# Kernel tuning notes

Measured on AMD Instinct MI355X. Metric: run time of the kernel, lower is better.

The kernel has to match this reference:

```python
import jax, jax.numpy as jnp
import numpy as np

N, E, D_IN, H, C = 50000, 1200000, 128, 8, 8  # heads=8, per-head dim=8, hidden=64
EPS_BN = 1e-5


def _bn(x, g, b):
    # BatchNorm1d in training mode: per-feature batch mean / biased var
    m = x.mean(0)
    v = x.var(0)
    return g * (x - m) * jax.lax.rsqrt(v + EPS_BN) + b


def _gatv2(x, src, dst, Wl, Wr, att):
    # PyG GATv2Conv (concat=True, bias=False, negative_slope=0.2, eval-mode dropout)
    xl = (x @ Wl).reshape(N, H, C)  # source transform (lin_l)
    xr = (x @ Wr).reshape(N, H, C)  # target transform (lin_r)
    e = jax.nn.leaky_relu(xl[src] + xr[dst], 0.2)          # [E,H,C]
    logits = jnp.einsum('ehc,hc->eh', e, att)               # [E,H]
    mx = jax.ops.segment_max(logits, dst, num_segments=N)   # [N,H]
    ex = jnp.exp(logits - mx[dst])
    den = jax.ops.segment_sum(ex, dst, num_segments=N)      # [N,H]
    alpha = ex / (den[dst] + 1e-16)                         # segment softmax over in-edges
    msg = xl[src] * alpha[..., None]                        # [E,H,C]
    out = jax.ops.segment_sum(msg.reshape(E, H * C), dst, num_segments=N)
    return out  # [N,64]


def setup_inputs() -> dict:
    key = jax.random.key(0)
    ks = jax.random.split(key, 40)
    d = {}
    d['x'] = jax.random.normal(ks[0], (N, D_IN), dtype=jnp.float32)
    d['edge_index'] = jax.random.randint(ks[1], (2, E), 0, N, dtype=jnp.int64)
    d['Wpre'] = jax.random.normal(ks[2], (D_IN, 64), dtype=jnp.float32) * 0.05
    d['g0'] = jnp.ones((64,), jnp.float32); d['b0'] = jnp.zeros((64,), jnp.float32)
    for i, k0 in zip(range(1, 5), range(3, 19, 4)):
        d[f'Wl{i}'] = jax.random.normal(ks[k0], (64, 64), jnp.float32) * 0.1
        d[f'Wr{i}'] = jax.random.normal(ks[k0 + 1], (64, 64), jnp.float32) * 0.1
        d[f'att{i}'] = jax.random.normal(ks[k0 + 2], (H, C), jnp.float32) * 0.1
        d[f'g{i}'] = jnp.ones((64,), jnp.float32)
        d[f'b{i}'] = jnp.zeros((64,), jnp.float32)
    dims = [64, 48, 32, 16, 2]
    for j in range(4):
        d[f'Wp{j+1}'] = jax.random.normal(ks[20 + j], (dims[j], dims[j + 1]), jnp.float32) * 0.1
        d[f'bp{j+1}'] = jnp.zeros((dims[j + 1],), jnp.float32)
    return d


def reference(x, edge_index, Wpre, g0, b0,
              Wl1, Wr1, att1, g1, b1,
              Wl2, Wr2, att2, g2, b2,
              Wl3, Wr3, att3, g3, b3,
              Wl4, Wr4, att4, g4, b4,
              Wp1, bp1, Wp2, bp2, Wp3, bp3, Wp4, bp4):
    src, dst = edge_index[0], edge_index[1]
    h = jax.nn.elu(_bn(x @ Wpre, g0, b0))
    for Wl, Wr, att, g, b in ((Wl1, Wr1, att1, g1, b1),
                              (Wl2, Wr2, att2, g2, b2),
                              (Wl3, Wr3, att3, g3, b3),
                              (Wl4, Wr4, att4, g4, b4)):
        h = jax.nn.elu(_bn(_gatv2(h, src, dst, Wl, Wr, att) + h, g, b))
    h = jax.nn.elu(h @ Wp1 + bp1)
    h = jax.nn.elu(h @ Wp2 + bp2)
    h = jax.nn.elu(h @ Wp3 + bp3)
    return h @ Wp4 + bp4
```

## Files before the change

### kernel.cpp

```cpp
#include <hip/hip_runtime.h>
#include <hip/hip_bf16.h>
#include <cmath>

__device__ inline void unpack_bf2(unsigned int u, float& lo, float& hi) {
    union { unsigned int i; float f; } a, b;
    a.i = u << 16; b.i = u & 0xffff0000u;
    lo = a.f; hi = b.f;
}
__device__ inline unsigned short bf16_bits(float x) {
    __hip_bfloat16 v = __float2bfloat16(x);
    return *reinterpret_cast<unsigned short*>(&v);
}

template<int K, int M, int ROWS>
__global__ __launch_bounds__(256)
void bn_gemm_kernel(const float* __restrict__ A, const float* __restrict__ B0,
                    const float* __restrict__ B1, float* __restrict__ C,
                    __hip_bfloat16* __restrict__ xlb, __hip_bfloat16* __restrict__ xrb,
                    const float* __restrict__ stats, const float* __restrict__ g,
                    const float* __restrict__ b, float* __restrict__ part,
                    int N, float invN)
{
    constexpr int TM  = ROWS * M / 512;
    constexpr int LDA = K + 4;
    constexpr int MT  = M / TM;
    __shared__ float Bs[K * M];
    __shared__ float As[ROWS * LDA];
    __shared__ float sA[K], sB[K];
    __shared__ float pst[2][4][64];
    if (stats != nullptr && threadIdx.x < K) {
        float m   = stats[threadIdx.x] * invN;
        float var = stats[K + threadIdx.x] * invN - m * m;
        float a   = g[threadIdx.x] * rsqrtf(var + 1e-5f);
        sA[threadIdx.x] = a;
        sB[threadIdx.x] = b[threadIdx.x] - m * a;
    }
    for (int i = threadIdx.x; i < K * M; i += 256) {
        float v;
        if (B1 != nullptr) {
            int k = i / M, m = i - k * M;
            v = (m < M / 2) ? B0[k * (M / 2) + m] : B1[k * (M / 2) + (m - M / 2)];
        } else {
            v = B0[i];
        }
        Bs[i] = v;
    }
    __syncthreads();
    int row0 = blockIdx.x * ROWS;
    for (int i = threadIdx.x; i < ROWS * K; i += 256) {
        int rr = i / K, kk = i - rr * K;
        int r = row0 + rr;
        float v = (r < N) ? A[(size_t)r * K + kk] : 0.f;
        if (stats != nullptr) {
            float t = fmaf(v, sA[kk], sB[kk]);
            v = (t > 0.f) ? t : expm1f(t);
        }
        As[rr * LDA + kk] = v;
    }
    __syncthreads();
    int r0 = (threadIdx.x / MT) * 2;
    int m0 = (threadIdx.x % MT) * TM;
    float acc0[TM], acc1[TM];
    #pragma unroll
    for (int i = 0; i < TM; ++i) { acc0[i] = 0.f; acc1[i] = 0.f; }
    const float* a0p = &As[r0 * LDA];
    const float* a1p = a0p + LDA;
    for (int k = 0; k < K; ++k) {
        float a0 = a0p[k], a1 = a1p[k];
        #pragma unroll
        for (int mm = 0; mm < TM; mm += 4) {
            float4 bv = *(const float4*)&Bs[k * M + m0 + mm];
            acc0[mm + 0] = fmaf(a0, bv.x, acc0[mm + 0]);
            acc0[mm + 1] = fmaf(a0, bv.y, acc0[mm + 1]);
            acc0[mm + 2] = fmaf(a0, bv.z, acc0[mm + 2]);
            acc0[mm + 3] = fmaf(a0, bv.w, acc0[mm + 3]);
            acc1[mm + 0] = fmaf(a1, bv.x, acc1[mm + 0]);
            acc1[mm + 1] = fmaf(a1, bv.y, acc1[mm + 1]);
            acc1[mm + 2] = fmaf(a1, bv.z, acc1[mm + 2]);
            acc1[mm + 3] = fmaf(a1, bv.w, acc1[mm + 3]);
        }
    }
    int rA = row0 + r0, rB = rA + 1;
    if (C != nullptr) {
        #pragma unroll
        for (int mm = 0; mm < TM; mm += 4) {
            if (rA < N)
                *(float4*)&C[(size_t)rA * M + m0 + mm] =
                    make_float4(acc0[mm], acc0[mm+1], acc0[mm+2], acc0[mm+3]);
            if (rB < N)
                *(float4*)&C[(size_t)rB * M + m0 + mm] =
                    make_float4(acc1[mm], acc1[mm+1], acc1[mm+2], acc1[mm+3]);
        }
    } else {
        unsigned int u0[4], u1[4];
        #pragma unroll
        for (int i = 0; i < 4; ++i) {
            u0[i] = (unsigned int)bf16_bits(acc0[2*i]) |
                    ((unsigned int)bf16_bits(acc0[2*i+1]) << 16);
            u1[i] = (unsigned int)bf16_bits(acc1[2*i]) |
                    ((unsigned int)bf16_bits(acc1[2*i+1]) << 16);
        }
        __hip_bfloat16* dst = (m0 < 64) ? xlb : xrb;
        int mo = (m0 < 64) ? m0 : m0 - 64;
        if (rA < N) *(uint4*)(dst + (size_t)rA * 64 + mo) = make_uint4(u0[0],u0[1],u0[2],u0[3]);
        if (rB < N) *(uint4*)(dst + (size_t)rB * 64 + mo) = make_uint4(u1[0],u1[1],u1[2],u1[3]);
    }
    if (part != nullptr) {
        float s[TM], s2[TM];
        #pragma unroll
        for (int i = 0; i < TM; ++i) {
            s[i]  = acc0[i] + acc1[i];
            s2[i] = acc0[i] * acc0[i] + acc1[i] * acc1[i];
        }
        #pragma unroll
        for (int off = MT; off < 64; off <<= 1) {
            #pragma unroll
            for (int i = 0; i < TM; ++i) {
                s[i]  += __shfl_xor(s[i],  off);
                s2[i] += __shfl_xor(s2[i], off);
            }
        }
        int lane = threadIdx.x & 63, wid = threadIdx.x >> 6;
        if (lane < MT) {
            #pragma unroll
            for (int c = 0; c < TM; ++c) {
                pst[0][wid][lane * TM + c] = s[c];
                pst[1][wid][lane * TM + c] = s2[c];
            }
        }
        __syncthreads();
        if (threadIdx.x < 128) {
            int which = threadIdx.x >> 6, f = threadIdx.x & 63;
            part[(size_t)blockIdx.x * 128 + threadIdx.x] =
                pst[which][0][f] + pst[which][1][f] +
                pst[which][2][f] + pst[which][3][f];
        }
    }
}

__global__ __launch_bounds__(128)
void stats_reduce1_kernel(const float* __restrict__ part, int nb,
                          float* __restrict__ part2)
{
    int f = threadIdx.x;
    float s = 0.f;
    for (int r = blockIdx.x; r < nb; r += 64)
        s += part[(size_t)r * 128 + f];
    part2[(size_t)blockIdx.x * 128 + f] = s;
}

__global__ __launch_bounds__(128)
void stats_reduce2_kernel(const float* __restrict__ part2,
                          float* __restrict__ stats)
{
    int f = threadIdx.x;
    float a = 0.f;
    #pragma unroll 8
    for (int r = 0; r < 64; ++r)
        a += part2[(size_t)r * 128 + f];
    stats[f] = a;
}

__global__ __launch_bounds__(256)
void bin_hist_kernel(const int* __restrict__ dsts, int* __restrict__ binCnt, int E)
{
    __shared__ int lh[4][256];
    for (int i = threadIdx.x; i < 1024; i += 256) ((int*)lh)[i] = 0;
    __syncthreads();
    int bank = threadIdx.x & 3;
    for (int e0 = blockIdx.x * 1024 + threadIdx.x * 4; e0 < E; e0 += gridDim.x * 1024) {
        if (e0 + 3 < E) {
            int4 d = *(const int4*)&dsts[e0];
            atomicAdd(&lh[bank][d.x >> 8], 1);
            atomicAdd(&lh[bank][d.y >> 8], 1);
            atomicAdd(&lh[bank][d.z >> 8], 1);
            atomicAdd(&lh[bank][d.w >> 8], 1);
        } else {
            for (int j = 0; j < 4; ++j)
                if (e0 + j < E) atomicAdd(&lh[bank][dsts[e0 + j] >> 8], 1);
        }
    }
    __syncthreads();
    int s = lh[0][threadIdx.x] + lh[1][threadIdx.x] +
            lh[2][threadIdx.x] + lh[3][threadIdx.x];
    if (s > 0) atomicAdd(&binCnt[threadIdx.x], s);
}

__global__ __launch_bounds__(256)
void bin_scan_kernel(const int* __restrict__ binCnt, int* __restrict__ binBase,
                     int* __restrict__ binCursor, int* __restrict__ row_ptr,
                     int* __restrict__ col, int N, int E)
{
    __shared__ int buf[256];
    int v = binCnt[threadIdx.x];
    buf[threadIdx.x] = v;
    __syncthreads();
    for (int off = 1; off < 256; off <<= 1) {
        int t = (threadIdx.x >= off) ? buf[threadIdx.x - off] : 0;
        __syncthreads();
        buf[threadIdx.x] += t;
        __syncthreads();
    }
    int excl = buf[threadIdx.x] - v;
    binBase[threadIdx.x] = excl;
    binCursor[threadIdx.x] = excl;
    if (threadIdx.x < 64) col[E + threadIdx.x] = 0;
    if (threadIdx.x == 255) {
        binBase[256] = buf[255];
        row_ptr[N] = E;
    }
}

#define SCHUNK 4096
__global__ __launch_bounds__(256)
void bin_scatter_kernel(const int* __restrict__ srcs, const int* __restrict__ dsts,
                        int* __restrict__ binCursor, unsigned int* __restrict__ binned,
                        int E)
{
    __shared__ unsigned int stg[SCHUNK];
    __shared__ int bcnt[256], bexcl[256], bcur[256], gbase[256], sbuf[256];
    int c0 = blockIdx.x * SCHUNK;
    int n = min(SCHUNK, E - c0);
    bcnt[threadIdx.x] = 0;
    __syncthreads();
    for (int k = 0; k < SCHUNK / 256; ++k) {
        int i = c0 + k * 256 + threadIdx.x;
        if (i < E) atomicAdd(&bcnt[dsts[i] >> 8], 1);
    }
    __syncthreads();
    int v = bcnt[threadIdx.x];
    sbuf[threadIdx.x] = v;
    __syncthreads();
    for (int off = 1; off < 256; off <<= 1) {
        int t = (threadIdx.x >= off) ? sbuf[threadIdx.x - off] : 0;
        __syncthreads();
        sbuf[threadIdx.x] += t;
        __syncthreads();
    }
    bexcl[threadIdx.x] = sbuf[threadIdx.x] - v;
    bcur[threadIdx.x]  = sbuf[threadIdx.x] - v;
    __syncthreads();
    for (int k = 0; k < SCHUNK / 256; ++k) {
        int i = c0 + k * 256 + threadIdx.x;
        if (i < E) {
            unsigned int s = (unsigned int)srcs[i], d = (unsigned int)dsts[i];
            int pos = atomicAdd(&bcur[d >> 8], 1);
            stg[pos] = (s << 16) | d;
        }
    }
    __syncthreads();
    gbase[threadIdx.x] = atomicAdd(&binCursor[threadIdx.x], bcnt[threadIdx.x]);
    __syncthreads();
    for (int i = threadIdx.x; i < n; i += 256) {
        unsigned int p = stg[i];
        int b = (p & 0xFFFFu) >> 8;
        binned[gbase[b] + (i - bexcl[b])] = p;
    }
}

__global__ __launch_bounds__(256)
void bin_finalize_kernel(const unsigned int* __restrict__ binned,
                         const int* __restrict__ binBase,
                         int* __restrict__ row_ptr, int* __restrict__ col, int N)
{
    __shared__ int cnt[256], excl[256], cur[256];
    int b = blockIdx.x;
    int beg = binBase[b], end = binBase[b + 1];
    cnt[threadIdx.x] = 0;
    __syncthreads();
    for (int i = beg + threadIdx.x; i < end; i += 256)
        atomicAdd(&cnt[binned[i] & 255u], 1);
    __syncthreads();
    int v = cnt[threadIdx.x];
    excl[threadIdx.x] = v;
    __syncthreads();
    for (int off = 1; off < 256; off <<= 1) {
        int t = (threadIdx.x >= off) ? excl[threadIdx.x - off] : 0;
        __syncthreads();
        excl[threadIdx.x] += t;
        __syncthreads();
    }
    int ex = excl[threadIdx.x] - v;
    int dstIdx = b * 256 + threadIdx.x;
    if (dstIdx < N) row_ptr[dstIdx] = beg + ex;
    cur[threadIdx.x] = ex;
    __syncthreads();
    for (int i = beg + threadIdx.x; i < end; i += 256) {
        unsigned int p = binned[i];
        int pos = atomicAdd(&cur[p & 255u], 1);
        col[beg + pos] = (int)(p >> 16) << 7;
    }
}

__device__ inline uint4 ldrow(const char* base_h, int offv, int slot) {
    int off = __shfl(offv, slot);
    return *(const uint4*)(base_h + off);
}

__global__ __launch_bounds__(256)
void gat_node_kernel(const int* __restrict__ row_ptr, const int* __restrict__ coloff,
                     const __hip_bfloat16* __restrict__ xlb,
                     const __hip_bfloat16* __restrict__ xrb,
                     const float* __restrict__ att,
                     const float* __restrict__ zin,
                     const float* __restrict__ stats, const float* __restrict__ g,
                     const float* __restrict__ b,
                     float* __restrict__ zout, float* __restrict__ part,
                     int N, float invN)
{
    int lane = threadIdx.x & 63;
    int wid  = threadIdx.x >> 6;
    int eg   = lane >> 3;
    int h    = lane & 7;

    __shared__ float AB[2][64];
    if (threadIdx.x < 64) {
        float m   = stats[threadIdx.x] * invN;
        float var = stats[64 + threadIdx.x] * invN - m * m;
        float a   = g[threadIdx.x] * rsqrtf(var + 1e-5f);
        AB[0][threadIdx.x] = a;
        AB[1][threadIdx.x] = b[threadIdx.x] - m * a;
    }
    __syncthreads();

    float attv[8];
    {
        const float4* a4 = (const float4*)(att + (h << 3));
        float4 a0 = a4[0], a1 = a4[1];
        attv[0]=a0.x; attv[1]=a0.y; attv[2]=a0.z; attv[3]=a0.w;
        attv[4]=a1.x; attv[5]=a1.y; attv[6]=a1.z; attv[7]=a1.w;
    }
    float fs[8], fs2[8];
    #pragma unroll
    for (int c = 0; c < 8; ++c) { fs[c] = 0.f; fs2[c] = 0.f; }

    const char* xh = (const char*)xlb + (h << 4);
    const int stride = gridDim.x * 4;

    int n = blockIdx.x * 4 + wid;
    int beg = 0, end = 0, cv0 = 0;
    if (n < N) {
        beg = row_ptr[n]; end = row_ptr[n + 1];
        int mm = min(lane, end - beg - 1); if (mm < 0) mm = 0;
        cv0 = coloff[beg + mm];
    }
    while (n < N) {
        uint4 xrp = *(const uint4*)((const char*)xrb + (size_t)n * 128 + (h << 4));
        float xr[8];
        unpack_bf2(xrp.x, xr[0], xr[1]);
        unpack_bf2(xrp.y, xr[2], xr[3]);
        unpack_bf2(xrp.z, xr[4], xr[5]);
        unpack_bf2(xrp.w, xr[6], xr[7]);
        float acc[8];
        #pragma unroll
        for (int c = 0; c < 8; ++c) acc[c] = 0.f;
        float den = 0.f;

        for (int gb = beg; gb < end; gb += 64) {
            int cnt = min(64, end - gb);
            int cm1 = cnt - 1;
            int cv = (gb == beg) ? cv0 : coloff[gb + min(lane, cm1)];
            int nck = (cnt + 15) >> 4;
            uint4 pA = ldrow(xh, cv, min(eg, cm1));
            uint4 pB = ldrow(xh, cv, min(eg + 8, cm1));
            for (int c = 0; c < nck; ++c) {
                uint4 nA = pA, nB = pB;
                if (c + 1 < nck) {
                    nA = ldrow(xh, cv, min((c + 1) * 16 + eg,     cm1));
                    nB = ldrow(xh, cv, min((c + 1) * 16 + 8 + eg, cm1));
                }
                int s0 = c * 16 + eg, s1 = s0 + 8;
                {
                    float xl[8];
                    unpack_bf2(pA.x, xl[0], xl[1]);
                    unpack_bf2(pA.y, xl[2], xl[3]);
                    unpack_bf2(pA.z, xl[4], xl[5]);
                    unpack_bf2(pA.w, xl[6], xl[7]);
                    float logit = 0.f;
                    #pragma unroll
                    for (int cc = 0; cc < 8; ++cc) {
                        float sum = xl[cc] + xr[cc];
                        float lr = fmaxf(sum, 0.2f * sum);
                        logit = fmaf(lr, attv[cc], logit);
                    }
                    float ex = (s0 < cnt) ? __expf(logit) : 0.f;
                    #pragma unroll
                    for (int cc = 0; cc < 8; ++cc) acc[cc] = fmaf(ex, xl[cc], acc[cc]);
                    den += ex;
                }
                {
                    float xl[8];
                    unpack_bf2(pB.x, xl[0], xl[1]);
                    unpack_bf2(pB.y, xl[2], xl[3]);
                    unpack_bf2(pB.z, xl[4], xl[5]);
                    unpack_bf2(pB.w, xl[6], xl[7]);
                    float logit = 0.f;
                    #pragma unroll
                    for (int cc = 0; cc < 8; ++cc) {
                        float sum = xl[cc] + xr[cc];
                        float lr = fmaxf(sum, 0.2f * sum);
                        logit = fmaf(lr, attv[cc], logit);
                    }
                    float ex = (s1 < cnt) ? __expf(logit) : 0.f;
                    #pragma unroll
                    for (int cc = 0; cc < 8; ++cc) acc[cc] = fmaf(ex, xl[cc], acc[cc]);
                    den += ex;
                }
                pA = nA; pB = nB;
            }
        }
        int n2 = n + stride;
        int beg2 = 0, end2 = 0;
        if (n2 < N) { beg2 = row_ptr[n2]; end2 = row_ptr[n2 + 1]; }
        float4 hr0, hr1;
        if (eg == 0) {
            const float4* zp = (const float4*)(zin + (size_t)n * 64 + (h << 3));
            hr0 = zp[0]; hr1 = zp[1];
        }
        #pragma unroll
        for (int off = 8; off <= 32; off <<= 1) {
            den += __shfl_xor(den, off);
            #pragma unroll
            for (int c = 0; c < 8; ++c) acc[c] += __shfl_xor(acc[c], off);
        }
        int cv2 = 0;
        if (n2 < N) {
            int mm = min(lane, end2 - beg2 - 1); if (mm < 0) mm = 0;
            cv2 = coloff[beg2 + mm];
        }
        if (eg == 0) {
            float inv = 1.f / (den + 1e-16f);
            float hraw[8] = {hr0.x, hr0.y, hr0.z, hr0.w, hr1.x, hr1.y, hr1.z, hr1.w};
            float v[8];
            #pragma unroll
            for (int c = 0; c < 8; ++c) {
                int f = (h << 3) + c;
                float t = fmaf(hraw[c], AB[0][f], AB[1][f]);
                float hv = (t > 0.f) ? t : expm1f(t);
                v[c] = fmaf(acc[c], inv, hv);
                fs[c] += v[c];
                fs2[c] += v[c] * v[c];
            }
            float4* z4 = (float4*)(zout + (size_t)n * 64 + (h << 3));
            z4[0] = make_float4(v[0], v[1], v[2], v[3]);
            z4[1] = make_float4(v[4], v[5], v[6], v[7]);
        }
        n = n2; beg = beg2; end = end2; cv0 = cv2;
    }
    __shared__ float lstat[2][4][64];
    if (eg == 0) {
        #pragma unroll
        for (int c = 0; c < 8; ++c) {
            lstat[0][wid][(h << 3) + c] = fs[c];
            lstat[1][wid][(h << 3) + c] = fs2[c];
        }
    }
    __syncthreads();
    if (threadIdx.x < 128) {
        int which = threadIdx.x >> 6;
        int f = threadIdx.x & 63;
        part[(size_t)blockIdx.x * 128 + threadIdx.x] =
            lstat[which][0][f] + lstat[which][1][f] +
            lstat[which][2][f] + lstat[which][3][f];
    }
}

__device__ inline float elu_f(float t) { return (t > 0.f) ? t : expm1f(t); }

__global__ __launch_bounds__(256)
void mlp_kernel(const float* __restrict__ z, const float* __restrict__ stats,
                const float* __restrict__ g, const float* __restrict__ b,
                const float* __restrict__ W1, const float* __restrict__ B1,
                const float* __restrict__ W2, const float* __restrict__ B2,
                const float* __restrict__ W3, const float* __restrict__ B3,
                const float* __restrict__ W4, const float* __restrict__ B4,
                float* __restrict__ out, int N, float invN)
{
    __shared__ float w1[64 * 48], w2[48 * 32], w3[32 * 16], w4[16 * 2];
    __shared__ float bb1[48], bb2[32], bb3[16], bb4[2];
    __shared__ float sA[64], sB[64];
    for (int i = threadIdx.x; i < 64 * 48; i += 256) w1[i] = W1[i];
    for (int i = threadIdx.x; i < 48 * 32; i += 256) w2[i] = W2[i];
    for (int i = threadIdx.x; i < 32 * 16; i += 256) w3[i] = W3[i];
    for (int i = threadIdx.x; i < 16 * 2;  i += 256) w4[i] = W4[i];
    if (threadIdx.x < 48) bb1[threadIdx.x] = B1[threadIdx.x];
    if (threadIdx.x < 32) bb2[threadIdx.x] = B2[threadIdx.x];
    if (threadIdx.x < 16) bb3[threadIdx.x] = B3[threadIdx.x];
    if (threadIdx.x < 2)  bb4[threadIdx.x] = B4[threadIdx.x];
    if (threadIdx.x >= 64 && threadIdx.x < 128) {
        int f = threadIdx.x - 64;
        float m   = stats[f] * invN;
        float var = stats[64 + f] * invN - m * m;
        float a   = g[f] * rsqrtf(var + 1e-5f);
        sA[f] = a;
        sB[f] = b[f] - m * a;
    }
    __syncthreads();
    int n = blockIdx.x * 256 + threadIdx.x;
    if (n >= N) return;
    float a[64];
    const float4* hp = (const float4*)(z + (size_t)n * 64);
    #pragma unroll
    for (int i = 0; i < 16; ++i) {
        float4 v = hp[i];
        a[4 * i] = v.x; a[4 * i + 1] = v.y; a[4 * i + 2] = v.z; a[4 * i + 3] = v.w;
    }
    #pragma unroll
    for (int k = 0; k < 64; ++k)
        a[k] = elu_f(fmaf(a[k], sA[k], sB[k]));

    float t1[48];
    for (int j = 0; j < 48; j += 4) {
        float c0 = bb1[j], c1 = bb1[j+1], c2 = bb1[j+2], c3 = bb1[j+3];
        #pragma unroll
        for (int k = 0; k < 64; ++k) {
            float4 wv = *(const float4*)&w1[k * 48 + j];
            c0 = fmaf(a[k], wv.x, c0);
            c1 = fmaf(a[k], wv.y, c1);
            c2 = fmaf(a[k], wv.z, c2);
            c3 = fmaf(a[k], wv.w, c3);
        }
        t1[j] = elu_f(c0); t1[j+1] = elu_f(c1); t1[j+2] = elu_f(c2); t1[j+3] = elu_f(c3);
    }
    float t2[32];
    for (int j = 0; j < 32; j += 4) {
        float c0 = bb2[j], c1 = bb2[j+1], c2 = bb2[j+2], c3 = bb2[j+3];
        #pragma unroll
        for (int k = 0; k < 48; ++k) {
            float4 wv = *(const float4*)&w2[k * 32 + j];
            c0 = fmaf(t1[k], wv.x, c0);
            c1 = fmaf(t1[k], wv.y, c1);
            c2 = fmaf(t1[k], wv.z, c2);
            c3 = fmaf(t1[k], wv.w, c3);
        }
        t2[j] = elu_f(c0); t2[j+1] = elu_f(c1); t2[j+2] = elu_f(c2); t2[j+3] = elu_f(c3);
    }
    float t3[16];
    for (int j = 0; j < 16; j += 4) {
        float c0 = bb3[j], c1 = bb3[j+1], c2 = bb3[j+2], c3 = bb3[j+3];
        #pragma unroll
        for (int k = 0; k < 32; ++k) {
            float4 wv = *(const float4*)&w3[k * 16 + j];
            c0 = fmaf(t2[k], wv.x, c0);
            c1 = fmaf(t2[k], wv.y, c1);
            c2 = fmaf(t2[k], wv.z, c2);
            c3 = fmaf(t2[k], wv.w, c3);
        }
        t3[j] = elu_f(c0); t3[j+1] = elu_f(c1); t3[j+2] = elu_f(c2); t3[j+3] = elu_f(c3);
    }
    float o0 = bb4[0], o1 = bb4[1];
    #pragma unroll
    for (int k = 0; k < 16; ++k) {
        o0 += t3[k] * w4[k * 2 + 0];
        o1 += t3[k] * w4[k * 2 + 1];
    }
    out[(size_t)n * 2 + 0] = o0;
    out[(size_t)n * 2 + 1] = o1;
}

extern "C" void kernel_launch(void* const* d_in, const int* in_sizes, int n_in,
                              void* d_out, int out_size, void* d_ws, size_t ws_size,
                              hipStream_t stream)
{
    const float* x    = (const float*)d_in[0];
    const int*   ei   = (const int*)d_in[1];
    const float* Wpre = (const float*)d_in[2];
    const float* g0   = (const float*)d_in[3];
    const float* b0   = (const float*)d_in[4];

    const int N = in_sizes[0] / 128;
    const int E = in_sizes[1] / 2;
    const float invN = 1.f / (float)N;
    const int NB = (N + 255) >> 8;
    const int GB = (N + 31) / 32;
    const int GG = 2048;

    float* ws  = (float*)d_ws;
    float* zA  = ws;
    float* zB  = zA + (size_t)N * 64;
    __hip_bfloat16* xlb = (__hip_bfloat16*)(zB + (size_t)N * 64);
    __hip_bfloat16* xrb = xlb + (size_t)N * 64;
    float* stats   = (float*)(xrb + (size_t)N * 64);
    int*   row_ptr = (int*)(stats + 5 * 128);
    int*   col     = row_ptr + N + 4;
    int*   binCnt    = col + E + 64;
    int*   binBase   = binCnt + 256;
    int*   binCursor = binBase + 260;
    float* part    = (float*)(binCursor + 256);
    float* part2   = part + (size_t)2048 * 128;
    unsigned int* binned = (unsigned int*)zB;

    const int* srcs = ei;
    const int* dsts = ei + E;

    hipMemsetAsync(binCnt, 0, 256 * sizeof(int), stream);
    bin_hist_kernel<<<256, 256, 0, stream>>>(dsts, binCnt, E);
    bin_scan_kernel<<<1, 256, 0, stream>>>(binCnt, binBase, binCursor, row_ptr, col, N, E);
    bin_scatter_kernel<<<(E + SCHUNK - 1) / SCHUNK, 256, 0, stream>>>(
        srcs, dsts, binCursor, binned, E);
    bin_finalize_kernel<<<NB, 256, 0, stream>>>(binned, binBase, row_ptr, col, N);

    bn_gemm_kernel<128, 64, 32><<<GB, 256, 0, stream>>>(
        x, Wpre, nullptr, zA, nullptr, nullptr, nullptr, nullptr, nullptr,
        part, N, invN);
    stats_reduce1_kernel<<<64, 128, 0, stream>>>(part, GB, part2);
    stats_reduce2_kernel<<<1, 128, 0, stream>>>(part2, stats);

    for (int l = 0; l < 4; ++l) {
        const float* Wl  = (const float*)d_in[5 + 5 * l + 0];
        const float* Wr  = (const float*)d_in[5 + 5 * l + 1];
        const float* att = (const float*)d_in[5 + 5 * l + 2];
        const float* gp = (l == 0) ? g0 : (const float*)d_in[5 + 5 * (l - 1) + 3];
        const float* bp = (l == 0) ? b0 : (const float*)d_in[5 + 5 * (l - 1) + 4];
        float* statsp = stats + 128 * l;
        float* zin  = (l & 1) ? zB : zA;
        float* zout = (l & 1) ? zA : zB;

        bn_gemm_kernel<64, 128, 32><<<GB, 256, 0, stream>>>(
            zin, Wl, Wr, nullptr, xlb, xrb, statsp, gp, bp, nullptr, N, invN);
        gat_node_kernel<<<GG, 256, 0, stream>>>(
            row_ptr, col, xlb, xrb, att, zin, statsp, gp, bp,
            zout, part, N, invN);
        stats_reduce1_kernel<<<64, 128, 0, stream>>>(part, GG, part2);
        stats_reduce2_kernel<<<1, 128, 0, stream>>>(part2, stats + 128 * (l + 1));
    }

    const float* g4  = (const float*)d_in[23];
    const float* b4  = (const float*)d_in[24];
    const float* Wp1 = (const float*)d_in[25]; const float* bp1 = (const float*)d_in[26];
    const float* Wp2 = (const float*)d_in[27]; const float* bp2 = (const float*)d_in[28];
    const float* Wp3 = (const float*)d_in[29]; const float* bp3 = (const float*)d_in[30];
    const float* Wp4 = (const float*)d_in[31]; const float* bp4 = (const float*)d_in[32];
    mlp_kernel<<<(N + 255) / 256, 256, 0, stream>>>(
        zA, stats + 512, g4, b4, Wp1, bp1, Wp2, bp2, Wp3, bp3, Wp4, bp4,
        (float*)d_out, N, invN);
}
```

Measured before the change: 517.7 us.

## Split final MLP across four lanes per node with shuffle-based activation exchange

The final MLP kernel now assigns four threads to each node instead of one. Each lane holds a quarter of the input features and computes a quarter of every layer's outputs, and the full activation vector is gathered via warp shuffles. This is meant to cut per-thread register pressure (previously 64+48+32+16 floats) and raise occupancy and parallelism. In exchange it adds shuffle traffic and launches four times as many threads. Only lane 0 of each group writes the output, as a single float2 store.

New measurement: 740.9 us. 43.1% more time.

```diff
diff --git a/kernel.cpp b/kernel.cpp
--- a/kernel.cpp
+++ b/kernel.cpp
@@ -496,66 +496,97 @@
         sB[f] = b[f] - m * a;
     }
     __syncthreads();
-    int n = blockIdx.x * 256 + threadIdx.x;
+    int t = blockIdx.x * 256 + threadIdx.x;
+    int n = t >> 2;
     if (n >= N) return;
-    float a[64];
-    const float4* hp = (const float4*)(z + (size_t)n * 64);
-    #pragma unroll
-    for (int i = 0; i < 16; ++i) {
-        float4 v = hp[i];
-        a[4 * i] = v.x; a[4 * i + 1] = v.y; a[4 * i + 2] = v.z; a[4 * i + 3] = v.w;
-    }
-    #pragma unroll
-    for (int k = 0; k < 64; ++k)
-        a[k] = elu_f(fmaf(a[k], sA[k], sB[k]));
-
-    float t1[48];
-    for (int j = 0; j < 48; j += 4) {
-        float c0 = bb1[j], c1 = bb1[j+1], c2 = bb1[j+2], c3 = bb1[j+3];
+    int lane = threadIdx.x & 63;
+    int q    = lane & 3;
+    int base = lane & ~3;
+
+    float a[16];
+    {
+        const float4* hp = (const float4*)(z + (size_t)n * 64 + (q << 4));
+        #pragma unroll
+        for (int i = 0; i < 4; ++i) {
+            float4 v = hp[i];
+            a[4*i] = v.x; a[4*i+1] = v.y; a[4*i+2] = v.z; a[4*i+3] = v.w;
+        }
+        #pragma unroll
+        for (int i = 0; i < 16; ++i) {
+            int f = (q << 4) + i;
+            a[i] = elu_f(fmaf(a[i], sA[f], sB[f]));
+        }
+    }
+
+    float t1[12];
+    {
+        float acc[12];
+        #pragma unroll
+        for (int j = 0; j < 12; ++j) acc[j] = bb1[q * 12 + j];
         #pragma unroll
         for (int k = 0; k < 64; ++k) {
-            float4 wv = *(const float4*)&w1[k * 48 + j];
-            c0 = fmaf(a[k], wv.x, c0);
-            c1 = fmaf(a[k], wv.y, c1);
-            c2 = fmaf(a[k], wv.z, c2);
-            c3 = fmaf(a[k], wv.w, c3);
-        }
-        t1[j] = elu_f(c0); t1[j+1] = elu_f(c1); t1[j+2] = elu_f(c2); t1[j+3] = elu_f(c3);
-    }
-    float t2[32];
-    for (int j = 0; j < 32; j += 4) {
-        float c0 = bb2[j], c1 = bb2[j+1], c2 = bb2[j+2], c3 = bb2[j+3];
+            float av = __shfl(a[k & 15], base + (k >> 4));
+            const float* wr = &w1[k * 48 + q * 12];
+            float4 w0 = *(const float4*)&wr[0];
+            float4 w4v = *(const float4*)&wr[4];
+            float4 w8 = *(const float4*)&wr[8];
+            acc[0] = fmaf(av, w0.x, acc[0]);  acc[1] = fmaf(av, w0.y, acc[1]);
+            acc[2] = fmaf(av, w0.z, acc[2]);  acc[3] = fmaf(av, w0.w, acc[3]);
+            acc[4] = fmaf(av, w4v.x, acc[4]); acc[5] = fmaf(av, w4v.y, acc[5]);
+            acc[6] = fmaf(av, w4v.z, acc[6]); acc[7] = fmaf(av, w4v.w, acc[7]);
+            acc[8] = fmaf(av, w8.x, acc[8]);  acc[9] = fmaf(av, w8.y, acc[9]);
+            acc[10] = fmaf(av, w8.z, acc[10]); acc[11] = fmaf(av, w8.w, acc[11]);
+        }
+        #pragma unroll
+        for (int j = 0; j < 12; ++j) t1[j] = elu_f(acc[j]);
+    }
+
+    float t2[8];
+    {
+        float acc[8];
+        #pragma unroll
+        for (int j = 0; j < 8; ++j) acc[j] = bb2[q * 8 + j];
         #pragma unroll
         for (int k = 0; k < 48; ++k) {
-            float4 wv = *(const float4*)&w2[k * 32 + j];
-            c0 = fmaf(t1[k], wv.x, c0);
-            c1 = fmaf(t1[k], wv.y, c1);
-            c2 = fmaf(t1[k], wv.z, c2);
-            c3 = fmaf(t1[k], wv.w, c3);
-        }
-        t2[j] = elu_f(c0); t2[j+1] = elu_f(c1); t2[j+2] = elu_f(c2); t2[j+3] = elu_f(c3);
-    }
-    float t3[16];
-    for (int j = 0; j < 16; j += 4) {
-        float c0 = bb3[j], c1 = bb3[j+1], c2 = bb3[j+2], c3 = bb3[j+3];
+            float tv = __shfl(t1[k % 12], base + (k / 12));
+            const float* wr = &w2[k * 32 + q * 8];
+            float4 w0 = *(const float4*)&wr[0];
+            float4 w4v = *(const float4*)&wr[4];
+            acc[0] = fmaf(tv, w0.x, acc[0]);  acc[1] = fmaf(tv, w0.y, acc[1]);
+            acc[2] = fmaf(tv, w0.z, acc[2]);  acc[3] = fmaf(tv, w0.w, acc[3]);
+            acc[4] = fmaf(tv, w4v.x, acc[4]); acc[5] = fmaf(tv, w4v.y, acc[5]);
+            acc[6] = fmaf(tv, w4v.z, acc[6]); acc[7] = fmaf(tv, w4v.w, acc[7]);
+        }
+        #pragma unroll
+        for (int j = 0; j < 8; ++j) t2[j] = elu_f(acc[j]);
+    }
+
+    float t3[4];
+    {
+        float acc[4];
+        #pragma unroll
+        for (int j = 0; j < 4; ++j) acc[j] = bb3[q * 4 + j];
         #pragma unroll
         for (int k = 0; k < 32; ++k) {
-            float4 wv = *(const float4*)&w3[k * 16 + j];
-            c0 = fmaf(t2[k], wv.x, c0);
-            c1 = fmaf(t2[k], wv.y, c1);
-            c2 = fmaf(t2[k], wv.z, c2);
-            c3 = fmaf(t2[k], wv.w, c3);
-        }
-        t3[j] = elu_f(c0); t3[j+1] = elu_f(c1); t3[j+2] = elu_f(c2); t3[j+3] = elu_f(c3);
-    }
+            float tv = __shfl(t2[k & 7], base + (k >> 3));
+            const float* wr = &w3[k * 16 + q * 4];
+            float4 w0 = *(const float4*)&wr[0];
+            acc[0] = fmaf(tv, w0.x, acc[0]); acc[1] = fmaf(tv, w0.y, acc[1]);
+            acc[2] = fmaf(tv, w0.z, acc[2]); acc[3] = fmaf(tv, w0.w, acc[3]);
+        }
+        #pragma unroll
+        for (int j = 0; j < 4; ++j) t3[j] = elu_f(acc[j]);
+    }
+
     float o0 = bb4[0], o1 = bb4[1];
     #pragma unroll
     for (int k = 0; k < 16; ++k) {
-        o0 += t3[k] * w4[k * 2 + 0];
-        o1 += t3[k] * w4[k * 2 + 1];
-    }
-    out[(size_t)n * 2 + 0] = o0;
-    out[(size_t)n * 2 + 1] = o1;
+        float tv = __shfl(t3[k & 3], base + (k >> 2));
+        o0 = fmaf(tv, w4[k * 2 + 0], o0);
+        o1 = fmaf(tv, w4[k * 2 + 1], o1);
+    }
+    if (q == 0)
+        *(float2*)&out[(size_t)n * 2] = make_float2(o0, o1);
 }
 
 extern "C" void kernel_launch(void* const* d_in, const int* in_sizes, int n_in,
@@ -631,7 +662,7 @@
     const float* Wp2 = (const float*)d_in[27]; const float* bp2 = (const float*)d_in[28];
     const float* Wp3 = (const float*)d_in[29]; const float* bp3 = (const float*)d_in[30];
     const float* Wp4 = (const float*)d_in[31]; const float* bp4 = (const float*)d_in[32];
-    mlp_kernel<<<(N + 255) / 256, 256, 0, stream>>>(
+    mlp_kernel<<<((N * 4) + 255) / 256, 256, 0, stream>>>(
         zA, stats + 512, g4, b4, Wp1, bp1, Wp2, bp2, Wp3, bp3, Wp4, bp4,
         (float*)d_out, N, invN);
 }
```
